# Kernel tuning notes

Hardware: AMD Instinct MI355X
Metric: run time of the kernel (lower is better)

## Reference

```python
import jax, jax.numpy as jnp
import numpy as np

B, N, D, H, G = 4, 2048, 384, 8, 512
K = 8            # knn neighbors (hardcoded in get_graph_feature)
HID = 4 * D      # mlp_ratio = 4
FIN = 3 + G      # fuse_mlp in_features


def _ln(x, g, b, eps=1e-5):
    m = x.mean(-1, keepdims=True)
    v = ((x - m) ** 2).mean(-1, keepdims=True)
    return (x - m) * jax.lax.rsqrt(v + eps) * g + b


def _self_attn(x, qkv_w, pw, pb):
    b, n, c = x.shape
    hd = c // H
    qkv = (x @ qkv_w).reshape(b, n, 3, H, hd).transpose(2, 0, 3, 1, 4)
    q, k, v = qkv[0], qkv[1], qkv[2]                      # [b,h,n,hd]
    a = jax.nn.softmax(jnp.einsum('bhnd,bhmd->bhnm', q, k) * hd ** -0.5, -1)
    o = jnp.einsum('bhnm,bhmd->bhnd', a, v).transpose(0, 2, 1, 3).reshape(b, n, c)
    return o @ pw + pb


def _cross_attn(q, v, qw, kw, vw, pw, pb):
    b, n, c = q.shape
    nk = v.shape[1]
    hd = c // H
    qh = (q @ qw).reshape(b, n, H, hd).transpose(0, 2, 1, 3)
    kh = (v @ kw).reshape(b, nk, H, hd).transpose(0, 2, 1, 3)
    vh = (v @ vw).reshape(b, nk, H, hd).transpose(0, 2, 1, 3)
    a = jax.nn.softmax(jnp.einsum('bhnd,bhmd->bhnm', qh, kh) * hd ** -0.5, -1)
    o = jnp.einsum('bhnm,bhmd->bhnd', a, vh).transpose(0, 2, 1, 3).reshape(b, n, c)
    return o @ pw + pb


def _graph_feature(x, knn_index, x_q=None):
    b, n, c = x.shape
    nq = x_q.shape[1] if x_q is not None else n
    feat = x.reshape(b * n, c)[knn_index.reshape(-1)].reshape(b, K, nq, c)
    xq = (x_q if x_q is not None else x)[:, None, :, :]   # [b,1,nq,c]
    return jnp.concatenate([feat - xq, jnp.broadcast_to(xq, feat.shape)], -1)


def setup_inputs():
    key = jax.random.key(0)
    ks = iter(jax.random.split(key, 32))
    nrm = lambda shape: jax.random.normal(next(ks), shape, jnp.float32) * 0.02
    f32 = jnp.float32
    inp = {
        'q': jax.random.normal(next(ks), (B, D, N), f32),
        'in_pos': jax.random.normal(next(ks), (B, 3, N), f32),
        'guide_coding': jax.random.normal(next(ks), (B, G), f32),
        'norm1_g': jnp.ones((D,), f32), 'norm1_b': jnp.zeros((D,), f32),
        'qkv_w': nrm((D, 3 * D)),
        'sa_proj_w': nrm((D, D)), 'sa_proj_b': jnp.zeros((D,), f32),
        'normq_g': jnp.ones((D,), f32), 'normq_b': jnp.zeros((D,), f32),
        'fuse1_w': nrm((FIN, FIN)), 'fuse1_b': jnp.zeros((FIN,), f32),
        'fuse2_w': nrm((FIN, D)), 'fuse2_b': jnp.zeros((D,), f32),
        'normv_g': jnp.ones((D,), f32), 'normv_b': jnp.zeros((D,), f32),
        'ca_q_w': nrm((D, D)), 'ca_k_w': nrm((D, D)), 'ca_v_w': nrm((D, D)),
        'ca_proj_w': nrm((D, D)), 'ca_proj_b': jnp.zeros((D,), f32),
        'norm2_g': jnp.ones((D,), f32), 'norm2_b': jnp.zeros((D,), f32),
        'mlp1_w': nrm((D, HID)), 'mlp1_b': jnp.zeros((HID,), f32),
        'mlp2_w': nrm((HID, D)), 'mlp2_b': jnp.zeros((D,), f32),
        'knn_w': nrm((2 * D, D)), 'knn_b': jnp.zeros((D,), f32),
        'merge_w': nrm((2 * D, D)), 'merge_b': jnp.zeros((D,), f32),
        'knnx_w': nrm((2 * D, D)), 'knnx_b': jnp.zeros((D,), f32),
        'mergex_w': nrm((2 * D, D)), 'mergex_b': jnp.zeros((D,), f32),
        'self_knn_index': jax.random.randint(next(ks), (B, K, N), 0, B * N),
        'cross_knn_index': jax.random.randint(next(ks), (B, K, N), 0, B * N),
    }
    return inp


def reference(q, in_pos, guide_coding, norm1_g, norm1_b, qkv_w, sa_proj_w, sa_proj_b,
              normq_g, normq_b, fuse1_w, fuse1_b, fuse2_w, fuse2_b, normv_g, normv_b,
              ca_q_w, ca_k_w, ca_v_w, ca_proj_w, ca_proj_b, norm2_g, norm2_b,
              mlp1_w, mlp1_b, mlp2_w, mlp2_b, knn_w, knn_b, merge_w, merge_b,
              knnx_w, knnx_b, mergex_w, mergex_b, self_knn_index, cross_knn_index):
    npoints = in_pos.shape[2]
    q = q.transpose(0, 2, 1)                              # [B,N,D]
    norm_q = _ln(q, norm1_g, norm1_b)
    q_1 = _self_attn(norm_q, qkv_w, sa_proj_w, sa_proj_b)
    # build v from positions + broadcast guide coding
    gc = jnp.broadcast_to(guide_coding[:, :, None], (q.shape[0], G, npoints))
    v = jnp.concatenate([in_pos, gc], axis=1).transpose(0, 2, 1)  # [B,N,3+G]
    v = jax.nn.gelu(v @ fuse1_w + fuse1_b, approximate=False) @ fuse2_w + fuse2_b
    # self knn branch
    knn_f = _graph_feature(norm_q, self_knn_index)        # [B,K,N,2D]
    knn_f = jax.nn.leaky_relu(knn_f @ knn_w + knn_b, 0.2).max(axis=1)
    q_1 = jnp.concatenate([q_1, knn_f], -1) @ merge_w + merge_b
    q = q + q_1
    norm_q = _ln(q, normq_g, normq_b)
    norm_v = _ln(v, normv_g, normv_b)
    q_2 = _cross_attn(norm_q, norm_v, ca_q_w, ca_k_w, ca_v_w, ca_proj_w, ca_proj_b)
    # cross knn branch
    knn_f = _graph_feature(norm_v, cross_knn_index, norm_q)
    knn_f = jax.nn.leaky_relu(knn_f @ knnx_w + knnx_b, 0.2).max(axis=1)
    q_2 = jnp.concatenate([q_2, knn_f], -1) @ mergex_w + mergex_b
    q = q + q_2
    h = _ln(q, norm2_g, norm2_b)
    q = q + (jax.nn.gelu(h @ mlp1_w + mlp1_b, approximate=False) @ mlp2_w + mlp2_b)
    return q.transpose(0, 2, 1)                           # [B,D,N]
```

## Files before the change

kernel.cpp:

```cpp
#include <hip/hip_runtime.h>
#include <cstdint>
#include <cstddef>

#define B_ 4
#define N_ 2048
#define D_ 384
#define H_ 8
#define HD_ 48
#define G_ 512
#define K_ 8
#define HID_ 1536
#define FIN_ 515
#define FINP_ 520
#define M_ (B_*N_)
#define QSCALE 0.20823512f

typedef unsigned short u16;
typedef __attribute__((ext_vector_type(8))) short bf16x8;
typedef __attribute__((ext_vector_type(4))) float f32x4;

#define GLOAD16(gp, lp) __builtin_amdgcn_global_load_lds( \
    (const __attribute__((address_space(1))) void*)(gp), \
    (__attribute__((address_space(3))) void*)(lp), 16, 0, 0)

__device__ __forceinline__ u16 f2bf(float x){
  unsigned u = __builtin_bit_cast(unsigned, x);
  unsigned r = (u + 0x7fffu + ((u >> 16) & 1u)) >> 16;
  return (u16)r;
}
__device__ __forceinline__ float bf2f(u16 v){
  unsigned u = ((unsigned)v) << 16;
  return __builtin_bit_cast(float, u);
}
__device__ __forceinline__ float exp2_hw(float x){
  float r;
  asm("v_exp_f32 %0, %1" : "=v"(r) : "v"(x));
  return r;
}
__device__ __forceinline__ float gelu_f(float x){
  return 0.5f*x*(1.f + erff(x*0.70710678118654752f));
}

__global__ __launch_bounds__(256) void transpose_k(const float* __restrict__ in,
    float* __restrict__ out, int R, int C){
  __shared__ float tile[32][33];
  int b = blockIdx.z;
  int c0 = blockIdx.x<<5, r0 = blockIdx.y<<5;
  const float* ip = in + (size_t)b*R*C;
  float* op = out + (size_t)b*R*C;
  int tx = threadIdx.x, ty = threadIdx.y;
  #pragma unroll
  for (int i = ty; i < 32; i += 8)
    tile[i][tx] = ip[(size_t)(r0+i)*C + c0 + tx];
  __syncthreads();
  #pragma unroll
  for (int i = ty; i < 32; i += 8)
    op[(size_t)(c0+i)*R + r0 + tx] = tile[tx][i];
}

struct WJob { const float* src; u16* dst; int Kd, Nd, Kp, diff, nbx, blk0; };
struct WJobs { WJob j[16]; };

__global__ __launch_bounds__(256) void wtconv_all(WJobs J){
  int b = blockIdx.x, ji = 0;
  #pragma unroll
  for (int i=1;i<16;i++) if (b >= J.j[i].blk0) ji = i;
  WJob jb = J.j[ji];
  int local = b - jb.blk0;
  int bx = local % jb.nbx, by = local / jb.nbx;
  __shared__ float tile[32][33];
  int k0 = bx<<5, n0 = by<<5;
  int tx = threadIdx.x, ty = threadIdx.y;
  #pragma unroll
  for (int i = ty; i < 32; i += 8){
    int k = k0+i, n = n0+tx;
    float v = 0.f;
    if (k < jb.Kd && n < jb.Nd){
      v = jb.src[(size_t)k*jb.Nd + n];
      if (jb.diff) v = jb.src[(size_t)(k+jb.diff)*jb.Nd + n] - v;
    }
    tile[i][tx] = v;
  }
  __syncthreads();
  #pragma unroll
  for (int i = ty; i < 32; i += 8){
    int n = n0+i, k = k0+tx;
    if (n < jb.Nd && k < jb.Kp) jb.dst[(size_t)n*jb.Kp + k] = f2bf(tile[tx][i]);
  }
}

struct WP { const float *pw, *mwt, *pb, *mb2; u16* W; float* Bo; };
__global__ __launch_bounds__(256) void wprod_k(WP a, WP b){
  WP w = blockIdx.y ? b : a;
  int idx = blockIdx.x*256 + threadIdx.x;
  if (idx >= 385*384) return;
  int n = idx % 384, kk = idx / 384;
  float acc = 0.f;
  if (kk < 384){
    for (int j=0;j<384;j++) acc += w.pw[(size_t)kk*384+j] * w.mwt[(size_t)j*384+n];
    w.W[(size_t)n*768 + kk] = f2bf(acc);
  } else {
    for (int j=0;j<384;j++) acc += w.pb[j] * w.mwt[(size_t)j*384+n];
    w.Bo[n] = acc + w.mb2[n];
  }
}

__global__ __launch_bounds__(256) void biasfill_k(const float* __restrict__ knnb,
    const float* __restrict__ knnxb, float* __restrict__ bws){
  int i = blockIdx.x*256 + threadIdx.x;
  if (i < 2688){
    float v = 0.f;
    if (i >= 1536 && i < 1920) v = knnb[i-1536];
    else if (i >= 2304) v = knnxb[i-2304];
    bws[i] = v;
  }
}

__device__ __forceinline__ void ln_body(const float* xr, const float* g,
    const float* bta, u16* yr, float* sbuf, int t){
  float v0 = xr[t], v1 = xr[t+128], v2 = xr[t+256];
  float s = v0+v1+v2;
  #pragma unroll
  for (int off=32; off>0; off>>=1) s += __shfl_down(s, off, 64);
  int lane = t & 63, w = t >> 6;
  if (lane==0) sbuf[w] = s;
  __syncthreads();
  float mean = (sbuf[0]+sbuf[1]) * (1.f/(float)D_);
  float d0 = v0-mean, d1 = v1-mean, d2 = v2-mean;
  float s2 = d0*d0 + d1*d1 + d2*d2;
  #pragma unroll
  for (int off=32; off>0; off>>=1) s2 += __shfl_down(s2, off, 64);
  __syncthreads();
  if (lane==0) sbuf[w] = s2;
  __syncthreads();
  float inv = rsqrtf((sbuf[0]+sbuf[1])*(1.f/(float)D_) + 1e-5f);
  yr[t]     = f2bf(d0*inv*g[t]     + bta[t]);
  yr[t+128] = f2bf(d1*inv*g[t+128] + bta[t+128]);
  yr[t+256] = f2bf(d2*inv*g[t+256] + bta[t+256]);
}

__global__ __launch_bounds__(128) void ln_bf(const float* __restrict__ x,
    const float* __restrict__ g, const float* __restrict__ bta, u16* __restrict__ y){
  __shared__ float sbuf[2];
  int row = blockIdx.x;
  ln_body(x + (size_t)row*D_, g, bta, y + (size_t)row*D_, sbuf, threadIdx.x);
}

__global__ __launch_bounds__(128) void ln2_bf(const float* __restrict__ x0,
    const float* __restrict__ g0, const float* __restrict__ b0, u16* __restrict__ y0,
    const float* __restrict__ x1, const float* __restrict__ g1,
    const float* __restrict__ b1, u16* __restrict__ y1){
  __shared__ float sbuf[2];
  int row = blockIdx.x;
  if (row < M_)
    ln_body(x0 + (size_t)row*D_, g0, b0, y0 + (size_t)row*D_, sbuf, threadIdx.x);
  else {
    row -= M_;
    ln_body(x1 + (size_t)row*D_, g1, b1, y1 + (size_t)row*D_, sbuf, threadIdx.x);
  }
}

template<int ACT, int OUTBF, int ACCUM, int HASBIAS, int SCALEQ>
__global__ __launch_bounds__(512) void gemm8(const u16* __restrict__ A, int lda,
    const u16* __restrict__ Wt, int ldw, const float* __restrict__ bias,
    float* __restrict__ Cf, u16* __restrict__ Cb, int ldc, int Kd, int Nd, int Npad){
  __shared__ char Lmem[33280];
  u16* As = (u16*)Lmem;
  u16* Bs = As + 128*64;
  float* cred = (float*)Lmem;
  const int t = threadIdx.x;
  const int wv = t>>6, l = t&63;
  const int kg = wv>>2, wq = wv&3;
  const int wm = wq&1, wn = wq>>1;
  const int lr = l&15, ls = l>>4;
  const int bm = blockIdx.y<<7, bn = blockIdx.x<<6;
  f32x4 z4 = {0.f,0.f,0.f,0.f};
  f32x4 acc[4][2];
  #pragma unroll
  for (int mi=0;mi<4;mi++){ acc[mi][0]=z4; acc[mi][1]=z4; }
  const int Kup = (Kd+63)&~63;
  for (int k0=0; k0<Kup; k0+=64){
    #pragma unroll
    for (int i=0;i<2;i++){
      int g = t + (i<<9);
      int row = g>>3, slot = g&7;
      int kk = k0 + slot*8;
      float4 val = {0.f,0.f,0.f,0.f};
      if (kk < Kd) val = *reinterpret_cast<const float4*>(A + (size_t)(bm+row)*lda + kk);
      int ss = slot ^ (row&7);
      *reinterpret_cast<float4*>((char*)As + row*128 + ss*16) = val;
    }
    {
      int row = t>>3, slot = t&7;
      int kk = k0 + slot*8;
      int n = bn + row;
      float4 val = {0.f,0.f,0.f,0.f};
      if (n < Nd && kk < Kd) val = *reinterpret_cast<const float4*>(Wt + (size_t)n*ldw + kk);
      int ss = slot ^ (row&7);
      *reinterpret_cast<float4*>((char*)Bs + row*128 + ss*16) = val;
    }
    __syncthreads();
    bf16x8 af[4], bfr[2];
    #pragma unroll
    for (int mi=0;mi<4;mi++){
      int row = wm*64 + mi*16 + lr;
      int ss = (kg*4 + ls) ^ (row&7);
      af[mi] = *reinterpret_cast<bf16x8*>((char*)As + row*128 + ss*16);
    }
    #pragma unroll
    for (int ni=0;ni<2;ni++){
      int row = wn*32 + ni*16 + lr;
      int ss = (kg*4 + ls) ^ (row&7);
      bfr[ni] = *reinterpret_cast<bf16x8*>((char*)Bs + row*128 + ss*16);
    }
    #pragma unroll
    for (int mi=0;mi<4;mi++)
      #pragma unroll
      for (int ni=0;ni<2;ni++)
        acc[mi][ni] = __builtin_amdgcn_mfma_f32_16x16x32_bf16(af[mi], bfr[ni], acc[mi][ni], 0,0,0);
    __syncthreads();
  }
  if (kg == 1){
    #pragma unroll
    for (int mi=0;mi<4;mi++)
      #pragma unroll
      for (int ni=0;ni<2;ni++)
        #pragma unroll
        for (int r=0;r<4;r++){
          int row = wm*64 + mi*16 + ls*4 + r;
          int col = wn*32 + ni*16 + lr;
          cred[row*65 + col] = acc[mi][ni][r];
        }
  }
  __syncthreads();
  if (kg == 0){
    #pragma unroll
    for (int mi=0;mi<4;mi++){
      #pragma unroll
      for (int ni=0;ni<2;ni++){
        #pragma unroll
        for (int r=0;r<4;r++){
          int rl = wm*64 + mi*16 + ls*4 + r;
          int cl = wn*32 + ni*16 + lr;
          int row = bm + rl, col = bn + cl;
          float v = acc[mi][ni][r] + cred[rl*65 + cl];
          if (col < Nd){
            if (SCALEQ && col < 384) v *= QSCALE;
            if (HASBIAS) v += bias[col];
            if (ACT) v = gelu_f(v);
            if (OUTBF) Cb[(size_t)row*ldc + col] = f2bf(v);
            else if (ACCUM) Cf[(size_t)row*ldc + col] += v;
            else Cf[(size_t)row*ldc + col] = v;
          } else if (OUTBF && col < Npad){
            Cb[(size_t)row*ldc + col] = 0;
          }
        }
      }
    }
  }
}

__global__ __launch_bounds__(256) void vt_k(const u16* __restrict__ X, int ld,
                                            u16* __restrict__ Vt){
  __shared__ u16 tl[64][72];
  int bh = blockIdx.y, b = bh>>3, h = bh&7;
  int n0 = blockIdx.x<<6;
  #pragma unroll
  for (int i=0;i<2;i++){
    int g = threadIdx.x + (i<<8);
    if (g < 384){
      int r = g/6, c = (g - r*6)*8;
      *reinterpret_cast<float4*>(&tl[r][c]) =
        *reinterpret_cast<const float4*>(X + (size_t)(b*N_ + n0 + r)*ld + h*HD_ + c);
    }
  }
  __syncthreads();
  #pragma unroll
  for (int i=0;i<2;i++){
    int g = threadIdx.x + (i<<8);
    if (g < 384){
      int d = g % 48, sb = g / 48;
      int hf = (n0>>6)&1;
      int kt0 = n0 & ~127;
      size_t rowb = ((size_t)(bh*HD_+d))*N_ + kt0;
      int kA = hf*64 + sb*8;
      ushort4 va, vb;
      va.x = tl[sb*8+0][d]; va.y = tl[sb*8+1][d];
      va.z = tl[sb*8+2][d]; va.w = tl[sb*8+3][d];
      vb.x = tl[sb*8+4][d]; vb.y = tl[sb*8+5][d];
      vb.z = tl[sb*8+6][d]; vb.w = tl[sb*8+7][d];
      int uA = ((kA>>5)<<2) | ((kA>>2)&3);
      int pA = (((uA ^ (d&15)))<<3) + (((kA>>4)&1)<<2);
      int kB = kA + 4;
      int uB = ((kB>>5)<<2) | ((kB>>2)&3);
      int pB = (((uB ^ (d&15)))<<3) + (((kB>>4)&1)<<2);
      *reinterpret_cast<ushort4*>(Vt + rowb + pA) = va;
      *reinterpret_cast<ushort4*>(Vt + rowb + pB) = vb;
    }
  }
}

__global__ __launch_bounds__(256) void attn_mfma(const u16* __restrict__ Qp, int ldq,
    const u16* __restrict__ Kp, int ldk, const u16* __restrict__ Vt,
    u16* __restrict__ O, int ldo){
  __shared__ u16 Kls[128*64];
  __shared__ u16 Vls[48*128];
  const int t = threadIdx.x, wv = t>>6, l = t&63;
  const int lr = l&15, ls = l>>4;
  const int bh = blockIdx.y, bb = bh>>3, h = bh&7;
  const int q0 = blockIdx.x<<6;
  bf16x8 zf = {0,0,0,0,0,0,0,0};
  f32x4 z4 = {0.f,0.f,0.f,0.f};
  const size_t rowQ = ((size_t)(bb*N_ + q0 + wv*16 + lr))*ldq + h*HD_;
  bf16x8 qa0 = *reinterpret_cast<const bf16x8*>(Qp + rowQ + 8*ls);
  bf16x8 qa1 = (ls < 2) ? *reinterpret_cast<const bf16x8*>(Qp + rowQ + 32 + 8*ls) : zf;
  f32x4 oacc[3] = {z4, z4, z4};
  float mrun = -1.0e30f, lrun = 0.f;

  const u16* Kbase = Kp + (size_t)(bb*N_)*ldk + h*HD_;
  const u16* Vbase = Vt + (size_t)bh*HD_*N_;
  int kgo[4];
  #pragma unroll
  for (int i=0;i<4;i++){
    int g = t + (i<<8);
    int key = g>>3, s = g&7;
    kgo[i] = key*ldk + ((s ^ (key&7))<<3);
  }
  int vgo[3];
  #pragma unroll
  for (int i=0;i<3;i++){
    int g = t + (i<<8);
    int d = g>>4, s = g&15;
    vgo[i] = d*N_ + (s<<3);
  }

  for (int kt = 0; kt < N_/128; kt++){
    const u16* kp = Kbase + (size_t)kt*128*ldk;
    #pragma unroll
    for (int i=0;i<4;i++)
      GLOAD16(kp + kgo[i], (char*)Kls + ((t + (i<<8))<<4));
    const u16* vp = Vbase + kt*128;
    #pragma unroll
    for (int i=0;i<3;i++)
      GLOAD16(vp + vgo[i], (char*)Vls + ((t + (i<<8))<<4));
    __syncthreads();
    f32x4 S[8];
    __builtin_amdgcn_s_setprio(1);
    #pragma unroll
    for (int sub=0; sub<8; sub++){
      int krow = sub*16 + lr;
      bf16x8 kb0 = *reinterpret_cast<bf16x8*>((char*)Kls + krow*128 + ((ls ^ (krow&7))<<4));
      bf16x8 kb1 = *reinterpret_cast<bf16x8*>((char*)Kls + krow*128 + (((4+ls) ^ (krow&7))<<4));
      f32x4 s = __builtin_amdgcn_mfma_f32_16x16x32_bf16(kb0, qa0, z4, 0,0,0);
      S[sub] = __builtin_amdgcn_mfma_f32_16x16x32_bf16(kb1, qa1, s, 0,0,0);
    }
    __builtin_amdgcn_s_setprio(0);
    float tm = fmaxf(fmaxf(fmaxf(S[0][0],S[0][1]), fmaxf(S[0][2],S[0][3])),
                     fmaxf(fmaxf(S[1][0],S[1][1]), fmaxf(S[1][2],S[1][3])));
    #pragma unroll
    for (int sub=2;sub<8;sub++)
      tm = fmaxf(tm, fmaxf(fmaxf(S[sub][0],S[sub][1]), fmaxf(S[sub][2],S[sub][3])));
    if (__all(tm - mrun <= 10.f)){
      float ps = 0.f;
      #pragma unroll
      for (int sub=0;sub<8;sub++)
        #pragma unroll
        for (int r=0;r<4;r++){
          float p = exp2_hw(S[sub][r]-mrun);
          S[sub][r] = p; ps += p;
        }
      lrun += ps;
    } else {
      float mx = fmaxf(tm, __shfl_xor(tm, 16, 64));
      mx = fmaxf(mx, __shfl_xor(mx, 32, 64));
      float mnew = fmaxf(mrun, mx);
      float al = exp2_hw(mrun - mnew);
      mrun = mnew;
      float ps = 0.f;
      #pragma unroll
      for (int sub=0;sub<8;sub++)
        #pragma unroll
        for (int r=0;r<4;r++){
          float p = exp2_hw(S[sub][r]-mnew);
          S[sub][r] = p; ps += p;
        }
      lrun = lrun*al + ps;
      #pragma unroll
      for (int r=0;r<4;r++){
        float alq = __shfl(al, ls*4 + r, 64);
        oacc[0][r] *= alq; oacc[1][r] *= alq; oacc[2][r] *= alq;
      }
    }
    union PU { unsigned u[4]; bf16x8 v; };
    PU pa[4];
    #pragma unroll
    for (int kb=0;kb<4;kb++){
      asm("v_cvt_pk_bf16_f32 %0, %1, %2" : "=v"(pa[kb].u[0]) : "v"(S[2*kb][0]),   "v"(S[2*kb][1]));
      asm("v_cvt_pk_bf16_f32 %0, %1, %2" : "=v"(pa[kb].u[1]) : "v"(S[2*kb][2]),   "v"(S[2*kb][3]));
      asm("v_cvt_pk_bf16_f32 %0, %1, %2" : "=v"(pa[kb].u[2]) : "v"(S[2*kb+1][0]), "v"(S[2*kb+1][1]));
      asm("v_cvt_pk_bf16_f32 %0, %1, %2" : "=v"(pa[kb].u[3]) : "v"(S[2*kb+1][2]), "v"(S[2*kb+1][3]));
    }
    __builtin_amdgcn_s_setprio(1);
    #pragma unroll
    for (int ni=0;ni<3;ni++){
      int d = ni*16 + lr;
      #pragma unroll
      for (int kb=0;kb<4;kb++){
        bf16x8 vb = *reinterpret_cast<bf16x8*>((char*)Vls + d*256 + ((((kb*4+ls) ^ (d&15)))<<4));
        oacc[ni] = __builtin_amdgcn_mfma_f32_16x16x32_bf16(pa[kb].v, vb, oacc[ni], 0,0,0);
      }
    }
    __builtin_amdgcn_s_setprio(0);
    __syncthreads();
  }
  float sden = lrun;
  sden += __shfl_xor(sden, 16, 64);
  sden += __shfl_xor(sden, 32, 64);
  #pragma unroll
  for (int r=0;r<4;r++){
    float dq = __shfl(sden, ls*4 + r, 64);
    float inv = 1.f / dq;
    size_t orow = (size_t)(bb*N_ + q0 + wv*16 + ls*4 + r);
    #pragma unroll
    for (int ni=0;ni<3;ni++)
      O[orow*ldo + h*HD_ + ni*16 + lr] = f2bf(oacc[ni][r] * inv);
  }
}

__global__ __launch_bounds__(384) void gather_max_bf(const u16* __restrict__ P, int ldp,
    const u16* __restrict__ Q2, int ldq2, const int* __restrict__ idx,
    u16* __restrict__ out, int ldo){
  int m = blockIdx.x;
  int d = threadIdx.x;
  int b = m >> 11, n = m & (N_-1);
  float q2 = bf2f(Q2[(size_t)m*ldq2 + d]);
  float mx = -3.0e38f;
  #pragma unroll
  for (int k=0;k<K_;k++){
    int j = idx[((b<<3) + k)*N_ + n];
    float val = bf2f(P[(size_t)j*ldp + d]) + q2;
    val = (val >= 0.f) ? val : 0.2f*val;
    mx = fmaxf(mx, val);
  }
  out[(size_t)m*ldo + d] = f2bf(mx);
}

__global__ __launch_bounds__(256) void build_v(const float* __restrict__ pos,
    const float* __restrict__ gc, u16* __restrict__ v){
  int m = blockIdx.x;
  int b = m >> 11, n = m & (N_-1);
  for (int c = threadIdx.x; c < FINP_; c += 256){
    float val = 0.f;
    if (c < 3) val = pos[(b*3 + c)*N_ + n];
    else if (c < FIN_) val = gc[(b<<9) + (c-3)];
    v[(size_t)m*FINP_ + c] = f2bf(val);
  }
}

extern "C" void kernel_launch(void* const* d_in, const int* in_sizes, int n_in,
                              void* d_out, int out_size, void* d_ws, size_t ws_size,
                              hipStream_t stream){
  const float* q_in   = (const float*)d_in[0];
  const float* in_pos = (const float*)d_in[1];
  const float* guide  = (const float*)d_in[2];
  const float* n1g = (const float*)d_in[3];
  const float* n1b = (const float*)d_in[4];
  const float* qkv_w = (const float*)d_in[5];
  const float* sa_pw = (const float*)d_in[6];
  const float* sa_pb = (const float*)d_in[7];
  const float* nqg = (const float*)d_in[8];
  const float* nqb = (const float*)d_in[9];
  const float* f1w = (const float*)d_in[10];
  const float* f1b = (const float*)d_in[11];
  const float* f2w = (const float*)d_in[12];
  const float* f2b = (const float*)d_in[13];
  const float* nvg = (const float*)d_in[14];
  const float* nvb = (const float*)d_in[15];
  const float* caqw = (const float*)d_in[16];
  const float* cakw = (const float*)d_in[17];
  const float* cavw = (const float*)d_in[18];
  const float* capw = (const float*)d_in[19];
  const float* capb = (const float*)d_in[20];
  const float* n2g = (const float*)d_in[21];
  const float* n2b = (const float*)d_in[22];
  const float* m1w = (const float*)d_in[23];
  const float* m1b = (const float*)d_in[24];
  const float* m2w = (const float*)d_in[25];
  const float* m2b = (const float*)d_in[26];
  const float* knnw = (const float*)d_in[27];
  const float* knnb = (const float*)d_in[28];
  const float* mw = (const float*)d_in[29];
  const float* mb = (const float*)d_in[30];
  const float* knnxw = (const float*)d_in[31];
  const float* knnxb = (const float*)d_in[32];
  const float* mxw = (const float*)d_in[33];
  const float* mxb = (const float*)d_in[34];
  const int* sidx = (const int*)d_in[35];
  const int* cidx = (const int*)d_in[36];
  float* out = (float*)d_out;

  const size_t MD = (size_t)M_*D_;
  float* q_cur = (float*)d_ws;
  float* vbuf  = q_cur + MD;
  u16* R     = (u16*)(vbuf + MD);
  u16* nq_bf = R + (size_t)M_*1920;
  u16* nv_bf = nq_bf + MD;
  u16* cc    = nv_bf + MD;
  u16* vin   = cc + (size_t)M_*768;
  u16* e2    = vin + (size_t)M_*FINP_;
  u16* Vt    = e2 + (size_t)M_*FINP_;
  u16* wb    = Vt + (size_t)32*HD_*N_;
  u16* W1    = wb;  wb += (size_t)1920*384;
  u16* Wq    = wb;  wb += (size_t)768*384;
  u16* Wv    = wb;  wb += (size_t)1152*384;
  u16* Wfold = wb;  wb += (size_t)384*768;
  u16* Wfoldx= wb;  wb += (size_t)384*768;
  u16* f1T   = wb;  wb += (size_t)FIN_*FINP_;
  u16* f2T   = wb;  wb += (size_t)384*FINP_;
  u16* m1T   = wb;  wb += (size_t)1536*384;
  u16* m2T   = wb;  wb += (size_t)384*1536;
  if (((uintptr_t)wb & 3) != 0) wb++;
  float* bias_ws = (float*)wb;
  const size_t needed = (char*)(bias_ws + 3456) - (char*)d_ws;
  if (ws_size < needed) return;

  u16* X1 = R;
  u16* Xq = R;
  u16* Xv = R + (size_t)M_*768;
  u16* hid = R;

  dim3 tb32(32,8);
  transpose_k<<<dim3(N_/32, D_/32, B_), tb32, 0, stream>>>(q_in, q_cur, D_, N_);
  WJobs J;
  auto setj = [&](int i, const float* src, u16* dst, int Kd, int Nd, int Kp, int diff){
    J.j[i].src = src; J.j[i].dst = dst; J.j[i].Kd = Kd; J.j[i].Nd = Nd;
    J.j[i].Kp = Kp; J.j[i].diff = diff; J.j[i].nbx = (Kd+31)/32; J.j[i].blk0 = 0;
  };
  setj(0,  qkv_w, W1,                    384, 1152, 384, 0);
  setj(1,  knnw,  W1 + (size_t)1152*384, 384, 384, 384, 0);
  setj(2,  knnw,  W1 + (size_t)1536*384, 384, 384, 384, 384);
  setj(3,  caqw,  Wq,                    384, 384, 384, 0);
  setj(4,  knnxw, Wq + (size_t)384*384,  384, 384, 384, 384);
  setj(5,  cakw,  Wv,                    384, 384, 384, 0);
  setj(6,  cavw,  Wv + (size_t)384*384,  384, 384, 384, 0);
  setj(7,  knnxw, Wv + (size_t)768*384,  384, 384, 384, 0);
  setj(8,  mw  + (size_t)384*384, Wfold  + 384, 384, 384, 768, 0);
  setj(9,  mxw + (size_t)384*384, Wfoldx + 384, 384, 384, 768, 0);
  setj(10, f1w,   f1T, FIN_, FIN_, FINP_, 0);
  setj(11, f2w,   f2T, FIN_, 384, FINP_, 0);
  setj(12, m1w,   m1T, 384, 1536, 384, 0);
  setj(13, m2w,   m2T, 1536, 384, 1536, 0);
  int tot = 0;
  for (int i=0;i<14;i++){ J.j[i].blk0 = tot; tot += J.j[i].nbx * ((J.j[i].Nd+31)/32); }
  J.j[14] = J.j[13]; J.j[14].blk0 = 0x7fffffff; J.j[14].nbx = 1;
  J.j[15] = J.j[14];
  wtconv_all<<<tot, tb32, 0, stream>>>(J);
  WP wpa = { sa_pw, mw,  sa_pb, mb,  Wfold,  bias_ws + 2688 };
  WP wpb = { capw,  mxw, capb,  mxb, Wfoldx, bias_ws + 3072 };
  wprod_k<<<dim3(578, 2), 256, 0, stream>>>(wpa, wpb);
  biasfill_k<<<11, 256, 0, stream>>>(knnb, knnxb, bias_ws);
  ln_bf<<<M_, 128, 0, stream>>>(q_cur, n1g, n1b, nq_bf);
  gemm8<0,1,0,1,1><<<dim3(30, 64), 512, 0, stream>>>(nq_bf, 384, W1, 384, bias_ws, nullptr, X1, 1920, 384, 1920, 1920);
  vt_k<<<dim3(32, 32), 256, 0, stream>>>(X1 + 768, 1920, Vt);
  attn_mfma<<<dim3(32, 32), 256, 0, stream>>>(X1, 1920, X1 + 384, 1920, Vt, cc, 768);
  gather_max_bf<<<M_, 384, 0, stream>>>(X1 + 1152, 1920, X1 + 1536, 1920, sidx, cc + 384, 768);
  gemm8<0,0,1,1,0><<<dim3(6, 64), 512, 0, stream>>>(cc, 768, Wfold, 768, bias_ws + 2688, q_cur, nullptr, 384, 768, 384, 384);
  build_v<<<M_, 256, 0, stream>>>(in_pos, guide, vin);
  gemm8<1,1,0,1,0><<<dim3(9, 64), 512, 0, stream>>>(vin, FINP_, f1T, FINP_, f1b, nullptr, e2, FINP_, FIN_, FIN_, FINP_);
  gemm8<0,0,0,1,0><<<dim3(6, 64), 512, 0, stream>>>(e2, FINP_, f2T, FINP_, f2b, vbuf, nullptr, 384, FIN_, 384, 384);
  ln2_bf<<<2*M_, 128, 0, stream>>>(q_cur, nqg, nqb, nq_bf, vbuf, nvg, nvb, nv_bf);
  gemm8<0,1,0,1,1><<<dim3(12, 64), 512, 0, stream>>>(nq_bf, 384, Wq, 384, bias_ws + 1920, nullptr, Xq, 768, 384, 768, 768);
  gemm8<0,1,0,0,0><<<dim3(18, 64), 512, 0, stream>>>(nv_bf, 384, Wv, 384, nullptr, nullptr, Xv, 1152, 384, 1152, 1152);
  vt_k<<<dim3(32, 32), 256, 0, stream>>>(Xv + 384, 1152, Vt);
  attn_mfma<<<dim3(32, 32), 256, 0, stream>>>(Xq, 768, Xv, 1152, Vt, cc, 768);
  gather_max_bf<<<M_, 384, 0, stream>>>(Xv + 768, 1152, Xq + 384, 768, cidx, cc + 384, 768);
  gemm8<0,0,1,1,0><<<dim3(6, 64), 512, 0, stream>>>(cc, 768, Wfoldx, 768, bias_ws + 3072, q_cur, nullptr, 384, 768, 384, 384);
  ln_bf<<<M_, 128, 0, stream>>>(q_cur, n2g, n2b, nq_bf);
  gemm8<1,1,0,1,0><<<dim3(24, 64), 512, 0, stream>>>(nq_bf, 384, m1T, 384, m1b, nullptr, hid, 1536, 384, 1536, 1536);
  gemm8<0,0,1,1,0><<<dim3(6, 64), 512, 0, stream>>>(hid, 1536, m2T, 1536, m2b, q_cur, nullptr, 384, 1536, 384, 384);
  transpose_k<<<dim3(D_/32, N_/32, B_), tb32, 0, stream>>>(q_cur, out, N_, D_);
}
```

Before: 501.2 us.

## Double-buffer K/V tiles in attention kernel with async prefetch

Replaces the single K/V shared-memory tile with two buffers so the next tile's global-to-LDS loads are issued before computing on the current one. A partial vmcnt wait ensures only the current tile's loads have landed, and the loop barriers use raw s_barrier with scheduling fences. This aims to hide global memory latency behind the MFMA work, at the cost of doubling LDS use per block, which may reduce occupancy.

After: 490.7 us. 1.02x faster.

```diff
diff --git a/kernel.cpp b/kernel.cpp
--- a/kernel.cpp
+++ b/kernel.cpp
@@ -303,8 +303,7 @@
 __global__ __launch_bounds__(256) void attn_mfma(const u16* __restrict__ Qp, int ldq,
     const u16* __restrict__ Kp, int ldk, const u16* __restrict__ Vt,
     u16* __restrict__ O, int ldo){
-  __shared__ u16 Kls[128*64];
-  __shared__ u16 Vls[48*128];
+  __shared__ __align__(16) char KVls[2][28672];
   const int t = threadIdx.x, wv = t>>6, l = t&63;
   const int lr = l&15, ls = l>>4;
   const int bh = blockIdx.y, bb = bh>>3, h = bh&7;
@@ -334,23 +333,36 @@
     vgo[i] = d*N_ + (s<<3);
   }
 
+  auto stage = [&](int kt, char* buf){
+    const u16* kp = Kbase + (size_t)kt*128*ldk;
+    #pragma unroll
+    for (int i=0;i<4;i++)
+      GLOAD16(kp + kgo[i], buf + ((t + (i<<8))<<4));
+    const u16* vp = Vbase + kt*128;
+    #pragma unroll
+    for (int i=0;i<3;i++)
+      GLOAD16(vp + vgo[i], buf + 16384 + ((t + (i<<8))<<4));
+  };
+
+  stage(0, KVls[0]);
   for (int kt = 0; kt < N_/128; kt++){
-    const u16* kp = Kbase + (size_t)kt*128*ldk;
-    #pragma unroll
-    for (int i=0;i<4;i++)
-      GLOAD16(kp + kgo[i], (char*)Kls + ((t + (i<<8))<<4));
-    const u16* vp = Vbase + kt*128;
-    #pragma unroll
-    for (int i=0;i<3;i++)
-      GLOAD16(vp + vgo[i], (char*)Vls + ((t + (i<<8))<<4));
-    __syncthreads();
+    char* cbuf = KVls[kt&1];
+    if (kt+1 < N_/128){
+      stage(kt+1, KVls[(kt+1)&1]);
+      asm volatile("s_waitcnt vmcnt(7)" ::: "memory");
+    } else {
+      asm volatile("s_waitcnt vmcnt(0)" ::: "memory");
+    }
+    __builtin_amdgcn_sched_barrier(0);
+    __builtin_amdgcn_s_barrier();
+    __builtin_amdgcn_sched_barrier(0);
     f32x4 S[8];
     __builtin_amdgcn_s_setprio(1);
     #pragma unroll
     for (int sub=0; sub<8; sub++){
       int krow = sub*16 + lr;
-      bf16x8 kb0 = *reinterpret_cast<bf16x8*>((char*)Kls + krow*128 + ((ls ^ (krow&7))<<4));
-      bf16x8 kb1 = *reinterpret_cast<bf16x8*>((char*)Kls + krow*128 + (((4+ls) ^ (krow&7))<<4));
+      bf16x8 kb0 = *reinterpret_cast<bf16x8*>(cbuf + krow*128 + ((ls ^ (krow&7))<<4));
+      bf16x8 kb1 = *reinterpret_cast<bf16x8*>(cbuf + krow*128 + (((4+ls) ^ (krow&7))<<4));
       f32x4 s = __builtin_amdgcn_mfma_f32_16x16x32_bf16(kb0, qa0, z4, 0,0,0);
       S[sub] = __builtin_amdgcn_mfma_f32_16x16x32_bf16(kb1, qa1, s, 0,0,0);
     }
@@ -406,12 +418,14 @@
       int d = ni*16 + lr;
       #pragma unroll
       for (int kb=0;kb<4;kb++){
-        bf16x8 vb = *reinterpret_cast<bf16x8*>((char*)Vls + d*256 + ((((kb*4+ls) ^ (d&15)))<<4));
+        bf16x8 vb = *reinterpret_cast<bf16x8*>(cbuf + 16384 + d*256 + ((((kb*4+ls) ^ (d&15)))<<4));
         oacc[ni] = __builtin_amdgcn_mfma_f32_16x16x32_bf16(pa[kb].v, vb, oacc[ni], 0,0,0);
       }
     }
     __builtin_amdgcn_s_setprio(0);
-    __syncthreads();
+    __builtin_amdgcn_sched_barrier(0);
+    __builtin_amdgcn_s_barrier();
+    __builtin_amdgcn_sched_barrier(0);
   }
   float sden = lrun;
   sden += __shfl_xor(sden, 16, 64);
```
